# Kernel tuning notes

Hardware: AMD Instinct MI355X
Metric: run time of the kernel (lower is better)

## Reference

```python
import jax, jax.numpy as jnp
import numpy as np

B, S, D = 2, 2048, 1024
H, DK, DV = 16, 64, 64

def setup_inputs() -> dict:
    key = jax.random.key(0)
    ks = jax.random.split(key, 5)
    scale = 1.0 / np.sqrt(D)  # xavier-ish
    return {
        "Q": jax.random.normal(ks[0], (B, S, D), dtype=jnp.float32),
        "attn_mask": jax.random.uniform(ks[1], (B, S), dtype=jnp.float32),
        "W_Q": jax.random.normal(ks[2], (H * DK, D), dtype=jnp.float32) * scale,
        "b_Q": jnp.zeros((H * DK,), dtype=jnp.float32),
        "W_K": jax.random.normal(ks[3], (H * DK, D), dtype=jnp.float32) * scale,
        "b_K": jnp.zeros((H * DK,), dtype=jnp.float32),
        "W_V": jax.random.normal(ks[4], (H * DV, D), dtype=jnp.float32) * scale,
        "b_V": jnp.zeros((H * DV,), dtype=jnp.float32),
    }

def reference(Q, attn_mask, W_Q, b_Q, W_K, b_K, W_V, b_V):
    b, s, _ = Q.shape
    # projections -> [B, H, S, d]
    q = (Q @ W_Q.T + b_Q).reshape(b, s, H, DK).transpose(0, 2, 1, 3)
    k = (Q @ W_K.T + b_K).reshape(b, s, H, DK).transpose(0, 2, 1, 3)
    v = (Q @ W_V.T + b_V).reshape(b, s, H, DV).transpose(0, 2, 1, 3)
    # exp-based attention (NOT stable softmax), multiplicative mask
    scores = jnp.einsum('bhqd,bhkd->bhqk', q, k) / np.sqrt(DK)
    scores = jnp.exp(scores)
    # mask [B, S_key] broadcast over heads and queries -> [B, 1, 1, S]
    scores = scores * attn_mask[:, None, None, :]
    attn = scores / (jnp.sum(scores, axis=-1, keepdims=True) + 1e-8)
    context = jnp.einsum('bhqk,bhkd->bhqd', attn, v)
    # [B, H, S, DV] -> [B, S, H*DV]
    return context.transpose(0, 2, 1, 3).reshape(b, s, H * DV)
```

## Files before the change

kernel.cpp:

```cpp
#include <hip/hip_runtime.h>
#include <hip/hip_bf16.h>
#include <math.h>

#define BATCH  2
#define S_LEN  2048
#define DMODEL 1024
#define NH     16
#define DHEAD  64

typedef __attribute__((ext_vector_type(8))) short bf16x8;
typedef __attribute__((ext_vector_type(4))) float f32x4;

#define MFMA16(a,b,c) __builtin_amdgcn_mfma_f32_16x16x32_bf16((a),(b),(c),0,0,0)

#define QSCALE 0.18033688011110793f
#define EXP2F(x) __builtin_amdgcn_exp2f(x)

__device__ __forceinline__ unsigned int pkbf(float a, float b) {
    __hip_bfloat162 h = __float22bfloat162_rn(make_float2(a, b));
    union { __hip_bfloat162 h; unsigned int u; } v; v.h = h; return v.u;
}
__device__ __forceinline__ void gl2lds16(const void* g, void* l) {
    __builtin_amdgcn_global_load_lds(
        (const __attribute__((address_space(1))) void*)(g),
        (__attribute__((address_space(3))) void*)(l), 16, 0, 0);
}

__global__ __launch_bounds__(256) void cvt_all(
    const float* __restrict__ Q,  const float* __restrict__ WQ,
    const float* __restrict__ WK, const float* __restrict__ WV,
    const float* __restrict__ msk,
    unsigned short* __restrict__ Qbf, unsigned short* __restrict__ Wbf,
    unsigned short* __restrict__ mbf)
{
    int i = blockIdx.x * blockDim.x + threadIdx.x;
    const float* src;
    unsigned short* dst;
    int off;
    if (i < 524288) {
        src = Q; dst = Qbf; off = i;
    } else if (i < 917504) {
        int j = i - 524288;
        int which = j >> 17;
        src = (which == 0) ? WQ : ((which == 1) ? WK : WV);
        dst = Wbf + ((size_t)which << 20);
        off = j & 131071;
    } else {
        int j = i - 917504;
        if (j >= 512) return;
        src = msk; dst = mbf; off = j;
    }
    float4 a = ((const float4*)src)[2*off];
    float4 b = ((const float4*)src)[2*off + 1];
    uint4 o;
    o.x = pkbf(a.x, a.y); o.y = pkbf(a.z, a.w);
    o.z = pkbf(b.x, b.y); o.w = pkbf(b.z, b.w);
    ((uint4*)dst)[off] = o;
}

__global__ __launch_bounds__(256) void proj_mfma(
    const unsigned short* __restrict__ Abf,
    const unsigned short* __restrict__ Wbf,
    const float* __restrict__ bQ, const float* __restrict__ bK,
    const float* __restrict__ bV, const float* __restrict__ mask,
    unsigned short* __restrict__ qw, unsigned short* __restrict__ kw,
    unsigned short* __restrict__ vt)
{
    __shared__ union {
        struct { unsigned short At[2][128*64]; unsigned short Bt[2][128*64]; } s;
        unsigned short Ct[128*132];
    } sm;

    const int tid  = threadIdx.x;
    const int lane = tid & 63;
    const int wv   = tid >> 6;
    const int wm   = (wv >> 1) * 64;
    const int wn   = (wv & 1) * 64;
    const int q15  = lane & 15;
    const int quad = lane >> 4;

    const int f  = blockIdx.x + (blockIdx.y << 3) + (blockIdx.z << 8);
    const int l  = (f & 7) * 96 + (f >> 3);
    const int z  = l >> 8;
    const int lr = l & 255;
    const int n0 = (lr & 7) * 128;
    const int m0 = (lr >> 3) * 128;

    const unsigned short* Wz = Wbf + (size_t)z * DMODEL * DMODEL;
    const float* bias = (z == 0) ? bQ : ((z == 1) ? bK : bV);

    f32x4 zero4 = {0.f, 0.f, 0.f, 0.f};
    f32x4 acc[4][4];
    #pragma unroll
    for (int i = 0; i < 4; ++i)
        #pragma unroll
        for (int j = 0; j < 4; ++j) acc[i][j] = zero4;

    #define STAGE_PROJ(BUF, K0)                                                \
        _Pragma("unroll")                                                      \
        for (int c = 0; c < 4; ++c) {                                          \
            int o   = tid * 16 + c * 4096;                                     \
            int row = o >> 7;                                                  \
            int lb  = (o & 127) ^ ((row & 7) << 4);                            \
            gl2lds16(Abf + (size_t)(m0 + row) * DMODEL + (K0) + (lb >> 1),     \
                     (char*)sm.s.At[BUF] + o);                                 \
            gl2lds16(Wz  + (size_t)(n0 + row) * DMODEL + (K0) + (lb >> 1),     \
                     (char*)sm.s.Bt[BUF] + o);                                 \
        }

    STAGE_PROJ(0, 0)
    __syncthreads();

    const int sw = (q15 & 7) << 4;

    for (int t = 0; t < 16; ++t) {
        const int buf = t & 1;
        if (t < 15) { STAGE_PROJ(buf ^ 1, (t + 1) * 64) }

        bf16x8 af[4][2], bfr[4][2];
        #pragma unroll
        for (int i = 0; i < 4; ++i) {
            const char* pa = (const char*)sm.s.At[buf] + (wm + i*16 + q15) * 128;
            const char* pb = (const char*)sm.s.Bt[buf] + (wn + i*16 + q15) * 128;
            af[i][0]  = *(const bf16x8*)(pa + (( 0 + quad*16) ^ sw));
            af[i][1]  = *(const bf16x8*)(pa + ((64 + quad*16) ^ sw));
            bfr[i][0] = *(const bf16x8*)(pb + (( 0 + quad*16) ^ sw));
            bfr[i][1] = *(const bf16x8*)(pb + ((64 + quad*16) ^ sw));
        }

        if (z < 2) {
            #pragma unroll
            for (int ks = 0; ks < 2; ++ks)
                #pragma unroll
                for (int i = 0; i < 4; ++i)
                    #pragma unroll
                    for (int j = 0; j < 4; ++j)
                        acc[i][j] = MFMA16(bfr[j][ks], af[i][ks], acc[i][j]);
        } else {
            #pragma unroll
            for (int ks = 0; ks < 2; ++ks)
                #pragma unroll
                for (int i = 0; i < 4; ++i)
                    #pragma unroll
                    for (int j = 0; j < 4; ++j)
                        acc[i][j] = MFMA16(af[i][ks], bfr[j][ks], acc[i][j]);
        }
        __syncthreads();
    }
    #undef STAGE_PROJ

    if (z < 2) {
        const float qs = (z == 0) ? QSCALE : 1.0f;
        #pragma unroll
        for (int i = 0; i < 4; ++i) {
            int ml = wm + i*16 + q15;
            #pragma unroll
            for (int j = 0; j < 4; ++j) {
                int nl = wn + j*16 + quad*4;
                float4 b4 = *(const float4*)(bias + n0 + nl);
                f32x4 v = acc[i][j];
                uint2 u;
                u.x = pkbf((v.x + b4.x)*qs, (v.y + b4.y)*qs);
                u.y = pkbf((v.z + b4.z)*qs, (v.w + b4.w)*qs);
                *(uint2*)&sm.Ct[ml*132 + nl] = u;
            }
        }
    } else {
        #pragma unroll
        for (int i = 0; i < 4; ++i) {
            int ml = wm + i*16 + quad*4;
            int sg = m0 + ml;
            int b2 = sg >> 11, s0g = sg & 2047;
            float4 mk4 = *(const float4*)(mask + (size_t)b2*S_LEN + s0g);
            #pragma unroll
            for (int j = 0; j < 4; ++j) {
                int nl = wn + j*16 + q15;
                float bv = bias[n0 + nl];
                f32x4 v = acc[i][j];
                uint2 u;
                u.x = pkbf((v.x + bv)*mk4.x, (v.y + bv)*mk4.y);
                u.y = pkbf((v.z + bv)*mk4.z, (v.w + bv)*mk4.w);
                *(uint2*)&sm.Ct[nl*132 + ml] = u;
            }
        }
    }
    __syncthreads();

    {
        int row  = tid >> 1;
        int half = (tid & 1) * 64;
        const uint4* src = (const uint4*)&sm.Ct[row*132 + half];
        unsigned short* dst;
        if (z < 2) {
            unsigned short* outp = (z == 0) ? qw : kw;
            int mg = m0 + row;  int b2 = mg >> 11, s = mg & 2047;
            int n  = n0 + half; int hh = n >> 6;
            dst = outp + (((size_t)b2*NH + hh)*S_LEN + s)*DHEAD;
        } else {
            int n  = n0 + row;  int hh = n >> 6, dv = n & 63;
            int b2 = m0 >> 11, s0 = m0 & 2047;
            dst = vt + (((size_t)b2*NH + hh)*DHEAD + dv)*S_LEN + s0 + half;
        }
        #pragma unroll
        for (int c = 0; c < 8; ++c) ((uint4*)dst)[c] = src[c];
    }
}

__global__ __launch_bounds__(256, 2) void attn_mfma(
    const unsigned short* __restrict__ qw, const unsigned short* __restrict__ kw,
    const unsigned short* __restrict__ vt, const unsigned short* __restrict__ mbf,
    float* __restrict__ out)
{
    __shared__ __align__(16) unsigned short Ks[2][64][64];
    __shared__ __align__(16) unsigned short Vs[2][64][64];

    const int tid  = threadIdx.x;
    const int lane = tid & 63;
    const int wv   = tid >> 6;
    const int q15  = lane & 15;
    const int quad = lane >> 4;

    const int orig = blockIdx.x + (blockIdx.y << 4) + (blockIdx.z << 8);
    const int lid  = (orig & 7) * 64 + (orig >> 3);
    const int q0   = (lid & 15) * 128;
    const int head = lid >> 4;
    const int h    = head & 15;
    const int b    = head >> 4;

    const size_t headoff = ((size_t)b * NH + h) * S_LEN * DHEAD;
    const unsigned short* qb = qw + headoff;
    const unsigned short* kb = kw + headoff;
    const unsigned short* vb = vt + headoff;
    const unsigned short* mb = mbf + (size_t)b * S_LEN;

    bf16x8 qf[2][2];
    #pragma unroll
    for (int qi = 0; qi < 2; ++qi) {
        const unsigned short* qr = qb + (size_t)(q0 + wv*32 + qi*16 + q15)*DHEAD;
        qf[qi][0] = *(const bf16x8*)(qr + quad*8);
        qf[qi][1] = *(const bf16x8*)(qr + 32 + quad*8);
    }

    const int srow = tid >> 3;
    const int kap  = (srow & 3) | (((srow >> 4) & 1) << 2) | (((srow >> 2) & 3) << 3);
    const int lb   = ((tid & 7) * 16) ^ ((srow & 7) << 4);
    const unsigned short* ksrc0 = kb + (size_t)kap        * DHEAD + (lb >> 1);
    const unsigned short* ksrc1 = kb + (size_t)(kap + 32) * DHEAD + (lb >> 1);
    const unsigned short* vsrc0 = vb + (size_t)srow        * S_LEN + (lb >> 1);
    const unsigned short* vsrc1 = vb + (size_t)(srow + 32) * S_LEN + (lb >> 1);
    char* kdst = (char*)&Ks[0][0][0] + tid * 16;
    char* vdst = (char*)&Vs[0][0][0] + tid * 16;
    const int sw = (q15 & 7) << 4;

    f32x4 zero4 = {0.f, 0.f, 0.f, 0.f};
    f32x4 oacc[2][4];
    f32x4 dacc[2];
    #pragma unroll
    for (int qi = 0; qi < 2; ++qi) {
        dacc[qi] = zero4;
        #pragma unroll
        for (int nj = 0; nj < 4; ++nj) oacc[qi][nj] = zero4;
    }

    gl2lds16(ksrc0, kdst);
    gl2lds16(ksrc1, kdst + 4096);
    gl2lds16(vsrc0, vdst);
    gl2lds16(vsrc1, vdst + 4096);
    bf16x8 mc0 = *(const bf16x8*)(mb + quad*8);
    bf16x8 mc1 = *(const bf16x8*)(mb + 32 + quad*8);

    for (int t = 0; t < 32; ++t) {
        const int buf = t & 1;
        const int kn  = (t < 31) ? (t + 1) * 64 : 0;

        __syncthreads();

        if (t < 31) {
            const int ob = (buf ^ 1) * 8192;
            gl2lds16(ksrc0 + (size_t)kn * DHEAD, kdst + ob);
            gl2lds16(ksrc1 + (size_t)kn * DHEAD, kdst + ob + 4096);
            gl2lds16(vsrc0 + kn, vdst + ob);
            gl2lds16(vsrc1 + kn, vdst + ob + 4096);
        }
        bf16x8 mn0 = *(const bf16x8*)(mb + kn + quad*8);
        bf16x8 mn1 = *(const bf16x8*)(mb + kn + 32 + quad*8);

        const char* kbase = (const char*)&Ks[0][0][0] + buf * 8192;
        f32x4 s[2][4];
        __builtin_amdgcn_s_setprio(1);
        #pragma unroll
        for (int ks = 0; ks < 4; ++ks) {
            const char* krp = kbase + (ks*16 + q15) * 128;
            bf16x8 kf0 = *(const bf16x8*)(krp + (( 0 + quad*16) ^ sw));
            bf16x8 kf1 = *(const bf16x8*)(krp + ((64 + quad*16) ^ sw));
            #pragma unroll
            for (int qi = 0; qi < 2; ++qi) {
                f32x4 a = MFMA16(kf0, qf[qi][0], zero4);
                s[qi][ks] = MFMA16(kf1, qf[qi][1], a);
            }
        }
        __builtin_amdgcn_s_setprio(0);
        bf16x8 pf[2][2];
        #pragma unroll
        for (int qi = 0; qi < 2; ++qi) {
            uint4 u0, u1;
            u0.x = pkbf(EXP2F(s[qi][0][0]), EXP2F(s[qi][0][1]));
            u0.y = pkbf(EXP2F(s[qi][0][2]), EXP2F(s[qi][0][3]));
            u0.z = pkbf(EXP2F(s[qi][1][0]), EXP2F(s[qi][1][1]));
            u0.w = pkbf(EXP2F(s[qi][1][2]), EXP2F(s[qi][1][3]));
            u1.x = pkbf(EXP2F(s[qi][2][0]), EXP2F(s[qi][2][1]));
            u1.y = pkbf(EXP2F(s[qi][2][2]), EXP2F(s[qi][2][3]));
            u1.z = pkbf(EXP2F(s[qi][3][0]), EXP2F(s[qi][3][1]));
            u1.w = pkbf(EXP2F(s[qi][3][2]), EXP2F(s[qi][3][3]));
            union { uint4 u; bf16x8 h; } c0, c1;
            c0.u = u0; c1.u = u1;
            pf[qi][0] = c0.h;
            pf[qi][1] = c1.h;
        }
        const char* vbase = (const char*)&Vs[0][0][0] + buf * 8192;
        __builtin_amdgcn_s_setprio(1);
        #pragma unroll
        for (int qi = 0; qi < 2; ++qi) {
            dacc[qi] = MFMA16(pf[qi][0], mc0, dacc[qi]);
            dacc[qi] = MFMA16(pf[qi][1], mc1, dacc[qi]);
        }
        #pragma unroll
        for (int nj = 0; nj < 4; ++nj) {
            const char* vrp = vbase + (nj*16 + q15) * 128;
            bf16x8 vf0 = *(const bf16x8*)(vrp + (( 0 + quad*16) ^ sw));
            bf16x8 vf1 = *(const bf16x8*)(vrp + ((64 + quad*16) ^ sw));
            #pragma unroll
            for (int qi = 0; qi < 2; ++qi) {
                oacc[qi][nj] = MFMA16(pf[qi][0], vf0, oacc[qi][nj]);
                oacc[qi][nj] = MFMA16(pf[qi][1], vf1, oacc[qi][nj]);
            }
        }
        __builtin_amdgcn_s_setprio(0);
        mc0 = mn0; mc1 = mn1;
    }

    #pragma unroll
    for (int qi = 0; qi < 2; ++qi)
        #pragma unroll
        for (int r = 0; r < 4; ++r) {
            float inv = 1.0f / (dacc[qi][r] + 1e-8f);
            size_t row = ((size_t)b*S_LEN + q0 + wv*32 + qi*16 + quad*4 + r)*DMODEL
                       + h*DHEAD;
            #pragma unroll
            for (int nj = 0; nj < 4; ++nj)
                out[row + nj*16 + q15] = oacc[qi][nj][r] * inv;
        }
}

extern "C" void kernel_launch(void* const* d_in, const int* in_sizes, int n_in,
                              void* d_out, int out_size, void* d_ws, size_t ws_size,
                              hipStream_t stream) {
    const float* Q    = (const float*)d_in[0];
    const float* msk  = (const float*)d_in[1];
    const float* W_Q  = (const float*)d_in[2];
    const float* b_Q  = (const float*)d_in[3];
    const float* W_K  = (const float*)d_in[4];
    const float* b_K  = (const float*)d_in[5];
    const float* W_V  = (const float*)d_in[6];
    const float* b_V  = (const float*)d_in[7];
    float* out = (float*)d_out;

    unsigned short* wsu = (unsigned short*)d_ws;
    unsigned short* Qbf = wsu;
    unsigned short* Wbf = Qbf + (size_t)4096*1024;
    unsigned short* qwb = Wbf + (size_t)3*1024*1024;
    unsigned short* kwb = qwb + (size_t)4*1024*1024;
    unsigned short* vtb = kwb + (size_t)4*1024*1024;
    unsigned short* mbf = vtb + (size_t)4*1024*1024;

    cvt_all<<<3586, 256, 0, stream>>>(Q, W_Q, W_K, W_V, msk, Qbf, Wbf, mbf);

    proj_mfma<<<dim3(8, 32, 3), 256, 0, stream>>>(
        Qbf, Wbf, b_Q, b_K, b_V, msk, qwb, kwb, vtb);

    attn_mfma<<<dim3(S_LEN/128, NH, BATCH), 256, 0, stream>>>(
        qwb, kwb, vtb, mbf, out);
}
```

Before: 169.2 us.

## Software-pipeline attention loop: overlap previous tile's PV MFMAs with current exp

Restructures the attention main loop so that each iteration computes QK^T scores for tile t while issuing the P·V and denominator MFMAs for tile t-1, with the exp/bf16 packing done afterward. V fragments are loaded into registers early and P/V fragments are double-buffered in registers (A/B ping-pong), unrolled by two with a prologue and epilogue. The aim is to hide the exp/convert latency behind matrix work and to keep the MFMA pipe busier. The cost is higher register pressure from the extra live fragments, which could reduce occupancy.

Result: faster. 165.7 us (-2.1%).

```diff
diff --git a/kernel.cpp b/kernel.cpp
--- a/kernel.cpp
+++ b/kernel.cpp
@@ -262,81 +262,110 @@
         for (int nj = 0; nj < 4; ++nj) oacc[qi][nj] = zero4;
     }
 
+    bf16x8 pfA[2][2], pfB[2][2];
+    bf16x8 vfA[4][2], vfB[4][2];
+
+    #define ATTN_BODY(T, BUF, PFP, VFP, PFN, VFN, DOPV, DOPREF)                 \
+    {                                                                           \
+        const char* kbase = (const char*)&Ks[0][0][0] + (BUF) * 8192;           \
+        const char* vbase = (const char*)&Vs[0][0][0] + (BUF) * 8192;           \
+        _Pragma("unroll")                                                       \
+        for (int nj = 0; nj < 4; ++nj) {                                        \
+            const char* vrp = vbase + (nj*16 + q15) * 128;                      \
+            VFN[nj][0] = *(const bf16x8*)(vrp + (( 0 + quad*16) ^ sw));         \
+            VFN[nj][1] = *(const bf16x8*)(vrp + ((64 + quad*16) ^ sw));         \
+        }                                                                       \
+        if (DOPREF) {                                                           \
+            const int kn = ((T) + 1) * 64;                                      \
+            const int ob = ((BUF) ^ 1) * 8192;                                  \
+            gl2lds16(ksrc0 + (size_t)kn * DHEAD, kdst + ob);                    \
+            gl2lds16(ksrc1 + (size_t)kn * DHEAD, kdst + ob + 4096);             \
+            gl2lds16(vsrc0 + kn, vdst + ob);                                    \
+            gl2lds16(vsrc1 + kn, vdst + ob + 4096);                             \
+        }                                                                       \
+        bf16x8 mp0, mp1;                                                        \
+        if (DOPV) {                                                             \
+            mp0 = *(const bf16x8*)(mb + ((T)-1)*64 + quad*8);                   \
+            mp1 = *(const bf16x8*)(mb + ((T)-1)*64 + 32 + quad*8);              \
+        }                                                                       \
+        f32x4 s[2][4];                                                          \
+        __builtin_amdgcn_s_setprio(1);                                          \
+        _Pragma("unroll")                                                       \
+        for (int ks = 0; ks < 4; ++ks) {                                        \
+            const char* krp = kbase + (ks*16 + q15) * 128;                      \
+            bf16x8 kf0 = *(const bf16x8*)(krp + (( 0 + quad*16) ^ sw));         \
+            bf16x8 kf1 = *(const bf16x8*)(krp + ((64 + quad*16) ^ sw));         \
+            _Pragma("unroll")                                                   \
+            for (int qi = 0; qi < 2; ++qi) {                                    \
+                f32x4 a = MFMA16(kf0, qf[qi][0], zero4);                        \
+                s[qi][ks] = MFMA16(kf1, qf[qi][1], a);                          \
+            }                                                                   \
+        }                                                                       \
+        if (DOPV) {                                                             \
+            _Pragma("unroll")                                                   \
+            for (int qi = 0; qi < 2; ++qi) {                                    \
+                dacc[qi] = MFMA16(PFP[qi][0], mp0, dacc[qi]);                   \
+                dacc[qi] = MFMA16(PFP[qi][1], mp1, dacc[qi]);                   \
+            }                                                                   \
+            _Pragma("unroll")                                                   \
+            for (int nj = 0; nj < 4; ++nj)                                      \
+                _Pragma("unroll")                                               \
+                for (int qi = 0; qi < 2; ++qi) {                                \
+                    oacc[qi][nj] = MFMA16(PFP[qi][0], VFP[nj][0], oacc[qi][nj]);\
+                    oacc[qi][nj] = MFMA16(PFP[qi][1], VFP[nj][1], oacc[qi][nj]);\
+                }                                                               \
+        }                                                                       \
+        __builtin_amdgcn_s_setprio(0);                                          \
+        _Pragma("unroll")                                                       \
+        for (int qi = 0; qi < 2; ++qi) {                                        \
+            uint4 u0, u1;                                                       \
+            u0.x = pkbf(EXP2F(s[qi][0][0]), EXP2F(s[qi][0][1]));                \
+            u0.y = pkbf(EXP2F(s[qi][0][2]), EXP2F(s[qi][0][3]));                \
+            u0.z = pkbf(EXP2F(s[qi][1][0]), EXP2F(s[qi][1][1]));                \
+            u0.w = pkbf(EXP2F(s[qi][1][2]), EXP2F(s[qi][1][3]));                \
+            u1.x = pkbf(EXP2F(s[qi][2][0]), EXP2F(s[qi][2][1]));                \
+            u1.y = pkbf(EXP2F(s[qi][2][2]), EXP2F(s[qi][2][3]));                \
+            u1.z = pkbf(EXP2F(s[qi][3][0]), EXP2F(s[qi][3][1]));                \
+            u1.w = pkbf(EXP2F(s[qi][3][2]), EXP2F(s[qi][3][3]));                \
+            union { uint4 u; bf16x8 hh; } c0, c1;                               \
+            c0.u = u0; c1.u = u1;                                               \
+            PFN[qi][0] = c0.hh;                                                 \
+            PFN[qi][1] = c1.hh;                                                 \
+        }                                                                       \
+        __syncthreads();                                                        \
+    }
+
     gl2lds16(ksrc0, kdst);
     gl2lds16(ksrc1, kdst + 4096);
     gl2lds16(vsrc0, vdst);
     gl2lds16(vsrc1, vdst + 4096);
-    bf16x8 mc0 = *(const bf16x8*)(mb + quad*8);
-    bf16x8 mc1 = *(const bf16x8*)(mb + 32 + quad*8);
-
-    for (int t = 0; t < 32; ++t) {
-        const int buf = t & 1;
-        const int kn  = (t < 31) ? (t + 1) * 64 : 0;
-
-        __syncthreads();
-
-        if (t < 31) {
-            const int ob = (buf ^ 1) * 8192;
-            gl2lds16(ksrc0 + (size_t)kn * DHEAD, kdst + ob);
-            gl2lds16(ksrc1 + (size_t)kn * DHEAD, kdst + ob + 4096);
-            gl2lds16(vsrc0 + kn, vdst + ob);
-            gl2lds16(vsrc1 + kn, vdst + ob + 4096);
-        }
-        bf16x8 mn0 = *(const bf16x8*)(mb + kn + quad*8);
-        bf16x8 mn1 = *(const bf16x8*)(mb + kn + 32 + quad*8);
-
-        const char* kbase = (const char*)&Ks[0][0][0] + buf * 8192;
-        f32x4 s[2][4];
-        __builtin_amdgcn_s_setprio(1);
-        #pragma unroll
-        for (int ks = 0; ks < 4; ++ks) {
-            const char* krp = kbase + (ks*16 + q15) * 128;
-            bf16x8 kf0 = *(const bf16x8*)(krp + (( 0 + quad*16) ^ sw));
-            bf16x8 kf1 = *(const bf16x8*)(krp + ((64 + quad*16) ^ sw));
+    __syncthreads();
+
+    ATTN_BODY(0, 0, pfB, vfB, pfA, vfA, 0, 1)
+
+    for (int t = 1; t < 31; t += 2) {
+        ATTN_BODY(t,     1, pfA, vfA, pfB, vfB, 1, 1)
+        ATTN_BODY(t + 1, 0, pfB, vfB, pfA, vfA, 1, 1)
+    }
+
+    ATTN_BODY(31, 1, pfA, vfA, pfB, vfB, 1, 0)
+    #undef ATTN_BODY
+
+    {
+        bf16x8 mp0 = *(const bf16x8*)(mb + 31*64 + quad*8);
+        bf16x8 mp1 = *(const bf16x8*)(mb + 31*64 + 32 + quad*8);
+        #pragma unroll
+        for (int qi = 0; qi < 2; ++qi) {
+            dacc[qi] = MFMA16(pfB[qi][0], mp0, dacc[qi]);
+            dacc[qi] = MFMA16(pfB[qi][1], mp1, dacc[qi]);
+        }
+        #pragma unroll
+        for (int nj = 0; nj < 4; ++nj)
             #pragma unroll
             for (int qi = 0; qi < 2; ++qi) {
-                f32x4 a = MFMA16(kf0, qf[qi][0], zero4);
-                s[qi][ks] = MFMA16(kf1, qf[qi][1], a);
+                oacc[qi][nj] = MFMA16(pfB[qi][0], vfB[nj][0], oacc[qi][nj]);
+                oacc[qi][nj] = MFMA16(pfB[qi][1], vfB[nj][1], oacc[qi][nj]);
             }
-        }
-        __builtin_amdgcn_s_setprio(0);
-        bf16x8 pf[2][2];
-        #pragma unroll
-        for (int qi = 0; qi < 2; ++qi) {
-            uint4 u0, u1;
-            u0.x = pkbf(EXP2F(s[qi][0][0]), EXP2F(s[qi][0][1]));
-            u0.y = pkbf(EXP2F(s[qi][0][2]), EXP2F(s[qi][0][3]));
-            u0.z = pkbf(EXP2F(s[qi][1][0]), EXP2F(s[qi][1][1]));
-            u0.w = pkbf(EXP2F(s[qi][1][2]), EXP2F(s[qi][1][3]));
-            u1.x = pkbf(EXP2F(s[qi][2][0]), EXP2F(s[qi][2][1]));
-            u1.y = pkbf(EXP2F(s[qi][2][2]), EXP2F(s[qi][2][3]));
-            u1.z = pkbf(EXP2F(s[qi][3][0]), EXP2F(s[qi][3][1]));
-            u1.w = pkbf(EXP2F(s[qi][3][2]), EXP2F(s[qi][3][3]));
-            union { uint4 u; bf16x8 h; } c0, c1;
-            c0.u = u0; c1.u = u1;
-            pf[qi][0] = c0.h;
-            pf[qi][1] = c1.h;
-        }
-        const char* vbase = (const char*)&Vs[0][0][0] + buf * 8192;
-        __builtin_amdgcn_s_setprio(1);
-        #pragma unroll
-        for (int qi = 0; qi < 2; ++qi) {
-            dacc[qi] = MFMA16(pf[qi][0], mc0, dacc[qi]);
-            dacc[qi] = MFMA16(pf[qi][1], mc1, dacc[qi]);
-        }
-        #pragma unroll
-        for (int nj = 0; nj < 4; ++nj) {
-            const char* vrp = vbase + (nj*16 + q15) * 128;
-            bf16x8 vf0 = *(const bf16x8*)(vrp + (( 0 + quad*16) ^ sw));
-            bf16x8 vf1 = *(const bf16x8*)(vrp + ((64 + quad*16) ^ sw));
-            #pragma unroll
-            for (int qi = 0; qi < 2; ++qi) {
-                oacc[qi][nj] = MFMA16(pf[qi][0], vf0, oacc[qi][nj]);
-                oacc[qi][nj] = MFMA16(pf[qi][1], vf1, oacc[qi][nj]);
-            }
-        }
-        __builtin_amdgcn_s_setprio(0);
-        mc0 = mn0; mc1 = mn1;
     }
 
     #pragma unroll
```
